# Kernel optimization log

Hardware: AMD Instinct MI355X
Metric: run time of the kernel (lower is better)

The kernel has to match this reference:

```python
import jax, jax.numpy as jnp
import numpy as np

H = 128

def _gine_conv(x, ei, ea, w1, b1, w2, b2):
    # GINEConv (eps=0): out = MLP(x + sum_{j->i} relu(x_j + e_ji))
    src, dst = ei[0], ei[1]
    m = jax.nn.relu(x[src] + ea)                      # [E, H]
    agg = jax.ops.segment_sum(m, dst, num_segments=x.shape[0])
    h = x + agg
    return jax.nn.relu(h @ w1 + b1) @ w2 + b2

def _bn(x, gamma, beta, eps=1e-5):
    # BatchNorm1d over node dim, batch statistics (training mode)
    mu = jnp.mean(x, axis=0)
    var = jnp.mean((x - mu) ** 2, axis=0)
    return gamma * (x - mu) * jax.lax.rsqrt(var + eps) + beta

def _scatter_mean(vals, ids, mask, n):
    w = mask.astype(vals.dtype)
    s = jax.ops.segment_sum(vals * w[:, None], ids, num_segments=n)
    c = jax.ops.segment_sum(w, ids, num_segments=n)
    return s / jnp.maximum(c, 1.0)[:, None]


def setup_inputs() -> dict:
    key = jax.random.key(0)
    ks = jax.random.split(key, 20)
    Nf, Nt, S, K = 320000, 100000, 20000, 16
    Ei, Eg = 1280000, 800000
    sc = 1.0 / np.sqrt(H)
    inp = {}
    inp["h_flat"] = jax.random.normal(ks[0], (Nf, H), jnp.float32)
    inp["intra_ei"] = jax.random.randint(ks[1], (2, Ei), 0, Nf, jnp.int32)
    inp["ea_flat"] = jax.random.normal(ks[2], (Ei, H), jnp.float32)
    inp["valid"] = jnp.ones((Nf,), jnp.bool_)
    inp["node_ids"] = jax.random.randint(ks[3], (Nf,), 0, Nt, jnp.int32)
    inp["N_total"] = Nt
    inp["edge_index"] = jax.random.randint(ks[4], (2, Eg), 0, Nt, jnp.int32)
    inp["edge_attr"] = jax.random.normal(ks[5], (Eg, H), jnp.float32)
    inp["sub_batch"] = jax.random.randint(ks[6], (Nf,), 0, S, jnp.int32)
    inp["S"] = S
    inp["k"] = K
    inp["root_flat_idx"] = jax.random.randint(ks[7], (S,), 0, Nf, jnp.int32)
    inp["is_root"] = jnp.zeros((Nf,), jnp.bool_)
    # parameters
    inp["local_w1"] = jax.random.normal(ks[8], (H, H), jnp.float32) * sc
    inp["local_b1"] = jnp.zeros((H,), jnp.float32)
    inp["local_w2"] = jax.random.normal(ks[9], (H, H), jnp.float32) * sc
    inp["local_b2"] = jnp.zeros((H,), jnp.float32)
    inp["local_gamma"] = jnp.ones((H,), jnp.float32)
    inp["local_beta"] = jnp.zeros((H,), jnp.float32)
    inp["global_w1"] = jax.random.normal(ks[10], (H, H), jnp.float32) * sc
    inp["global_b1"] = jnp.zeros((H,), jnp.float32)
    inp["global_w2"] = jax.random.normal(ks[11], (H, H), jnp.float32) * sc
    inp["global_b2"] = jnp.zeros((H,), jnp.float32)
    inp["global_gamma"] = jnp.ones((H,), jnp.float32)
    inp["global_beta"] = jnp.zeros((H,), jnp.float32)
    inp["skip_w"] = jax.random.normal(ks[12], (H, H), jnp.float32) * sc
    inp["skip_b"] = jnp.zeros((H,), jnp.float32)
    inp["vv_w"] = jax.random.normal(ks[13], (H, H), jnp.float32) * sc
    inp["vv_b"] = jnp.zeros((H,), jnp.float32)
    inp["kk_w"] = jax.random.normal(ks[14], (H, H), jnp.float32) * sc
    inp["kk_b"] = jnp.zeros((H,), jnp.float32)
    return inp


def reference(h_flat, intra_ei, ea_flat, valid, node_ids, N_total, edge_index, edge_attr,
              sub_batch, S, k, root_flat_idx, is_root,
              local_w1, local_b1, local_w2, local_b2, local_gamma, local_beta,
              global_w1, global_b1, global_w2, global_b2, global_gamma, global_beta,
              skip_w, skip_b, vv_w, vv_b, kk_w, kk_b):
    valid_f = valid.astype(h_flat.dtype)[:, None]
    clamped_ids = jnp.maximum(node_ids, 0)
    valid_mask = node_ids >= 0

    h_skip = (h_flat @ skip_w + skip_b) * valid_f

    h1 = _gine_conv(h_flat, intra_ei, ea_flat, local_w1, local_b1, local_w2, local_b2)
    h1 = _bn(h1, local_gamma, local_beta) * valid_f

    x_sum = _scatter_mean(h_flat, clamped_ids, valid_mask, N_total)   # [N_total, H]
    h2 = _gine_conv(x_sum, edge_index, edge_attr, global_w1, global_b1, global_w2, global_b2)
    h2 = _bn(h2, global_gamma, global_beta)[clamped_ids] * valid_f

    root_ids = node_ids[root_flat_idx]
    root_valid = root_ids >= 0
    x_vv_canonical = _scatter_mean(h_flat[root_flat_idx], jnp.maximum(root_ids, 0), root_valid, N_total)
    x_vv = (x_vv_canonical[clamped_ids] @ vv_w + vv_b) * valid_f

    x_kk = (h_flat[root_flat_idx[sub_batch]] @ kk_w + kk_b) * valid_f

    out = jax.nn.relu(h_skip + h1 + h2 + x_vv + x_kk)
    # dropout p=0.0 -> identity
    return out * valid_f
```

## Files before the change

kernel.cpp:

```cpp
#include <hip/hip_runtime.h>

#define H    128
#define HQ   32
#define TM   64
#define NT   100000
#define XS   136


typedef __attribute__((ext_vector_type(8))) short short8;
typedef __attribute__((ext_vector_type(4))) float f32x4;

static __host__ int cdiv(long a, long b) { return (int)((a + b - 1) / b); }
static __host__ char* alignp(char* p) {
    return (char*)(((uintptr_t)p + 255) & ~(uintptr_t)255);
}

__device__ inline unsigned short f2bf(float f) {
    unsigned u = __float_as_uint(f);
    unsigned r = u + 0x7FFFu + ((u >> 16) & 1u);
    return (unsigned short)(r >> 16);
}
__device__ inline float bf2f(unsigned short u) {
    return __uint_as_float((unsigned)u << 16);
}

struct WJobs { const float* src[7]; };

__global__ __launch_bounds__(256) void k_cvt_all(
    const float* __restrict__ in, unsigned short* __restrict__ out, long n8,
    WJobs wj, unsigned short* __restrict__ dstBase, int nCvt)
{
    if ((int)blockIdx.x < nCvt) {
        long i = (long)blockIdx.x * 256 + threadIdx.x;
        if (i >= n8) return;
        float4 a = ((const float4*)in)[2 * i];
        float4 b = ((const float4*)in)[2 * i + 1];
        ushort4 lo; lo.x = f2bf(a.x); lo.y = f2bf(a.y); lo.z = f2bf(a.z); lo.w = f2bf(a.w);
        ushort4 hi; hi.x = f2bf(b.x); hi.y = f2bf(b.y); hi.z = f2bf(b.z); hi.w = f2bf(b.w);
        ((ushort4*)out)[2 * i]     = lo;
        ((ushort4*)out)[2 * i + 1] = hi;
    } else {
        int b = blockIdx.x - nCvt;
        int w = b >> 4, chunk = b & 15;
        int i = chunk * 256 + threadIdx.x;
        int k = i >> 5, n4 = (i & 31) * 4;
        float4 v = ((const float4*)wj.src[w])[i];
        unsigned short* dst = dstBase + (size_t)w * H * H;
        dst[(n4 + 0) * H + k] = f2bf(v.x);
        dst[(n4 + 1) * H + k] = f2bf(v.y);
        dst[(n4 + 2) * H + k] = f2bf(v.z);
        dst[(n4 + 3) * H + k] = f2bf(v.w);
    }
}

struct CsrJobs {
    const int* ids[4];
    const int* srcarr[4];
    const int* rfi;
    int* cnt[4];
    int* rp[4];
    int* cur[4];
    int* eid[4];
    int2* pair[4];
    int  E[4];
    int  N[4];
    int  histBase[5];
    int  scanBase[5];
};

__device__ inline int csr_id(const CsrJobs& jb, int sg, int e)
{
    if (sg == 3) {
        int nid = jb.ids[2][jb.rfi[e]];
        return nid > 0 ? nid : 0;
    }
    return jb.ids[sg][e];
}

__global__ __launch_bounds__(256) void k_hist4(CsrJobs jb)
{
    int b = blockIdx.x, sg = 0;
    while (b >= jb.histBase[sg + 1]) ++sg;
    int e = (b - jb.histBase[sg]) * 256 + threadIdx.x;
    if (e < jb.E[sg]) atomicAdd(&jb.cnt[sg][csr_id(jb, sg, e)], 1);
}

__global__ __launch_bounds__(256) void k_scanA4(CsrJobs jb, int* __restrict__ parts)
{
    int b = blockIdx.x, sg = 0;
    while (b >= jb.scanBase[sg + 1]) ++sg;
    int lb = b - jb.scanBase[sg];
    const int* cnt = jb.cnt[sg];
    int* rowptr = jb.rp[sg];
    int N = jb.N[sg];
    int* partials = parts + sg * 256;

    __shared__ int lsum[256];
    int tid = threadIdx.x;
    int base = lb * 2048 + tid * 8;
    int v[8];
    int tsum = 0;
#pragma unroll
    for (int i = 0; i < 8; ++i) {
        int idx = base + i;
        int t = (idx < N) ? cnt[idx] : 0;
        v[i] = tsum;
        tsum += t;
    }
    lsum[tid] = tsum;
    __syncthreads();
    for (int off = 1; off < 256; off <<= 1) {
        int t = (tid >= off) ? lsum[tid - off] : 0;
        __syncthreads();
        lsum[tid] += t;
        __syncthreads();
    }
    int texcl = lsum[tid] - tsum;
#pragma unroll
    for (int i = 0; i < 8; ++i) {
        int idx = base + i;
        if (idx < N) rowptr[idx] = v[i] + texcl;
    }
    if (tid == 255) partials[lb] = lsum[255];
}

__global__ __launch_bounds__(256) void k_scanB4(CsrJobs jb, int* __restrict__ parts)
{
    int sg = blockIdx.x;
    int P = jb.scanBase[sg + 1] - jb.scanBase[sg];
    int* partials = parts + sg * 256;
    int* rowptr = jb.rp[sg];
    int N = jb.N[sg];

    __shared__ int lsum[256];
    int tid = threadIdx.x;
    int val = (tid < P) ? partials[tid] : 0;
    lsum[tid] = val;
    __syncthreads();
    for (int off = 1; off < 256; off <<= 1) {
        int t = (tid >= off) ? lsum[tid - off] : 0;
        __syncthreads();
        lsum[tid] += t;
        __syncthreads();
    }
    if (tid < P) partials[tid] = lsum[tid] - val;
    if (tid == 255) rowptr[N] = lsum[255];
}

__global__ __launch_bounds__(256) void k_scanC4(CsrJobs jb, const int* __restrict__ parts)
{
    int b = blockIdx.x, sg = 0;
    while (b >= jb.scanBase[sg + 1]) ++sg;
    int lb = b - jb.scanBase[sg];
    int off = parts[sg * 256 + lb];
    int N = jb.N[sg];
    int* rowptr = jb.rp[sg];
    int* cursor = jb.cur[sg];
    int base = lb * 2048;
    for (int i = threadIdx.x; i < 2048; i += 256) {
        int g = base + i;
        if (g < N) {
            int v = rowptr[g] + off;
            rowptr[g] = v;
            cursor[g] = v;
        }
    }
}

__global__ __launch_bounds__(256) void k_fillperm4(CsrJobs jb)
{
    int b = blockIdx.x, sg = 0;
    while (b >= jb.histBase[sg + 1]) ++sg;
    int e = (b - jb.histBase[sg]) * 256 + threadIdx.x;
    if (e < jb.E[sg]) {
        int pos = atomicAdd(&jb.cur[sg][csr_id(jb, sg, e)], 1);
        if (jb.srcarr[sg]) jb.pair[sg][pos] = make_int2(e, jb.srcarr[sg][e]);
        else               jb.eid[sg][pos] = e;
    }
}

__global__ __launch_bounds__(256) void k_csr_mean(
    const unsigned short* __restrict__ X, const int* __restrict__ eid,
    const int* __restrict__ rowptr, unsigned short* __restrict__ OUT, int N)
{
    int idx = blockIdx.x * 256 + threadIdx.x;
    int n = idx >> 5, l = idx & 31;
    if (n >= N) return;
    int beg = rowptr[n], end = rowptr[n + 1];
    float4 acc = {0.f, 0.f, 0.f, 0.f};
    for (int c0 = beg; c0 < end; c0 += 32) {
        int cnt = min(32, end - c0);
        int f_l = 0;
        if (l < cnt) f_l = eid[c0 + l];
        for (int j = 0; j < cnt; ++j) {
            int fi = __shfl(f_l, j, 32);
            ushort4 h = ((const ushort4*)(X + (size_t)fi * H))[l];
            acc.x += bf2f(h.x); acc.y += bf2f(h.y);
            acc.z += bf2f(h.z); acc.w += bf2f(h.w);
        }
    }
    float inv = 1.0f / fmaxf((float)(end - beg), 1.0f);
    ushort4 o;
    o.x = f2bf(acc.x * inv); o.y = f2bf(acc.y * inv);
    o.z = f2bf(acc.z * inv); o.w = f2bf(acc.w * inv);
    ((ushort4*)(OUT + (size_t)n * H))[l] = o;
}

__device__ inline void stage_x_copy(
    unsigned short* sX, const unsigned short* X1, const int* gidx,
    int r0, int M, int tid)
{
    int r = tid >> 2, q = tid & 3;
    int row = r0 + r;
    unsigned short* dst = &sX[r * XS + q * 32];
    if (row < M) {
        int sr = gidx ? gidx[row] : row;
        const ushort4* xp = (const ushort4*)(X1 + (size_t)sr * H + q * 32);
#pragma unroll
        for (int i = 0; i < 8; ++i) *(ushort4*)(dst + i * 4) = xp[i];
    } else {
#pragma unroll
        for (int i = 0; i < 8; ++i) *(ushort4*)(dst + i * 4) = ushort4{0, 0, 0, 0};
    }
}

__device__ inline void stage_wt_pre(
    unsigned short* sWT, const unsigned short* WT, int tid)
{
    for (int i = tid; i < H * HQ; i += 256) {
        int n = i >> 5, kq = i & 31;
        *(ushort4*)&sWT[n * XS + kq * 4] = ((const ushort4*)WT)[i];
    }
}

__device__ inline void stage_wt_half(
    unsigned short* sWT, const unsigned short* WT, int h, int tid)
{
    for (int i = tid; i < 64 * HQ; i += 256) {
        int n = i >> 5, kq = i & 31;
        *(ushort4*)&sWT[n * XS + kq * 4] = ((const ushort4*)WT)[h * 2048 + i];
    }
}

__global__ __launch_bounds__(256) void k_gemm(
    const unsigned short* __restrict__ X1, const int* __restrict__ gidx,
    const unsigned short* __restrict__ WT, const float* __restrict__ B,
    unsigned short* __restrict__ OUT, int M)
{
    __shared__ unsigned short sX[TM * XS];
    __shared__ unsigned short sWT[H * XS];
    __shared__ float sB[H];
    int tid = threadIdx.x;
    int r0 = blockIdx.x * TM;

    stage_x_copy(sX, X1, gidx, r0, M, tid);
    stage_wt_pre(sWT, WT, tid);
    if (tid < 32) ((float4*)sB)[tid] = ((const float4*)B)[tid];
    __syncthreads();

    int wv = tid >> 6, l = tid & 63;
    int lr = l & 15, hi = l >> 4, lk = hi * 8;

    f32x4 acc[8];
#pragma unroll
    for (int ct = 0; ct < 8; ++ct) acc[ct] = {0.f, 0.f, 0.f, 0.f};
#pragma unroll
    for (int kk = 0; kk < 4; ++kk) {
        short8 a = *(const short8*)&sX[(wv * 16 + lr) * XS + kk * 32 + lk];
#pragma unroll
        for (int ct = 0; ct < 8; ++ct) {
            short8 b = *(const short8*)&sWT[(ct * 16 + lr) * XS + kk * 32 + lk];
            acc[ct] = __builtin_amdgcn_mfma_f32_16x16x32_bf16(a, b, acc[ct], 0, 0, 0);
        }
    }

    int orow0 = r0 + wv * 16 + hi * 4;
#pragma unroll
    for (int ct = 0; ct < 8; ++ct) {
        int col = ct * 16 + lr;
        float bias = sB[col];
#pragma unroll
        for (int j = 0; j < 4; ++j) {
            int row = orow0 + j;
            if (row >= M) continue;
            OUT[(size_t)row * H + col] = f2bf(acc[ct][j] + bias);
        }
    }
}

__global__ __launch_bounds__(256) void k_mean_gemm(
    const unsigned short* __restrict__ X, const int* __restrict__ eid,
    const int* __restrict__ rowmap, const int* __restrict__ rowptr,
    const unsigned short* __restrict__ WT, const float* __restrict__ B,
    unsigned short* __restrict__ OUT, int M)
{
    __shared__ unsigned short sX[TM * XS];
    __shared__ unsigned short sWT[H * XS];
    __shared__ float sB[H];
    int tid = threadIdx.x;
    int r0 = blockIdx.x * TM;

    {
        int r = tid >> 2, q = tid & 3;
        int row = r0 + r;
        float4 m[8];
#pragma unroll
        for (int i = 0; i < 8; ++i) m[i] = {0.f, 0.f, 0.f, 0.f};
        int cnt = 0;
        if (row < M) {
            int beg = rowptr[row], end = rowptr[row + 1];
            cnt = end - beg;
            for (int j = beg; j < end; ++j) {
                int fi = rowmap[eid[j]];
                const ushort4* hp = (const ushort4*)(X + (size_t)fi * H + q * 32);
#pragma unroll
                for (int i = 0; i < 8; ++i) {
                    ushort4 v = hp[i];
                    m[i].x += bf2f(v.x); m[i].y += bf2f(v.y);
                    m[i].z += bf2f(v.z); m[i].w += bf2f(v.w);
                }
            }
        }
        float inv = 1.0f / fmaxf((float)cnt, 1.0f);
        unsigned short* dst = &sX[r * XS + q * 32];
#pragma unroll
        for (int i = 0; i < 8; ++i) {
            ushort4 b;
            b.x = f2bf(m[i].x * inv); b.y = f2bf(m[i].y * inv);
            b.z = f2bf(m[i].z * inv); b.w = f2bf(m[i].w * inv);
            *(ushort4*)(dst + i * 4) = b;
        }
    }
    stage_wt_pre(sWT, WT, tid);
    if (tid < 32) ((float4*)sB)[tid] = ((const float4*)B)[tid];
    __syncthreads();

    int wv = tid >> 6, l = tid & 63;
    int lr = l & 15, hi = l >> 4, lk = hi * 8;

    f32x4 acc[8];
#pragma unroll
    for (int ct = 0; ct < 8; ++ct) acc[ct] = {0.f, 0.f, 0.f, 0.f};
#pragma unroll
    for (int kk = 0; kk < 4; ++kk) {
        short8 a = *(const short8*)&sX[(wv * 16 + lr) * XS + kk * 32 + lk];
#pragma unroll
        for (int ct = 0; ct < 8; ++ct) {
            short8 b = *(const short8*)&sWT[(ct * 16 + lr) * XS + kk * 32 + lk];
            acc[ct] = __builtin_amdgcn_mfma_f32_16x16x32_bf16(a, b, acc[ct], 0, 0, 0);
        }
    }

    int orow0 = r0 + wv * 16 + hi * 4;
#pragma unroll
    for (int ct = 0; ct < 8; ++ct) {
        int col = ct * 16 + lr;
        float bias = sB[col];
#pragma unroll
        for (int j = 0; j < 4; ++j) {
            int row = orow0 + j;
            if (row >= M) continue;
            OUT[(size_t)row * H + col] = f2bf(acc[ct][j] + bias);
        }
    }
}

__global__ __launch_bounds__(256) void k_mlp_agg(
    const unsigned short* __restrict__ X1,
    const float* __restrict__ EA,
    const int2* __restrict__ pair,
    const int* __restrict__ rowptr,
    const unsigned short* __restrict__ W1T, const float* __restrict__ B1,
    const unsigned short* __restrict__ W2T, const float* __restrict__ B2,
    unsigned short* __restrict__ OUT, int M,
    float* __restrict__ gs, float* __restrict__ gs2)
{
    __shared__ unsigned short sX[TM * XS];
    __shared__ unsigned short sWT[64 * XS];
    __shared__ float sB1[H], sB2[H];
    __shared__ float sS[H], sS2[H];
    int tid = threadIdx.x;
    int r0 = blockIdx.x * TM;

    {
        int r = tid >> 2, q = tid & 3;
        int row = r0 + r;
        unsigned short* dst = &sX[r * XS + q * 32];
        if (row < M) {
            float4 m[8];
            const ushort4* xp = (const ushort4*)(X1 + (size_t)row * H + q * 32);
#pragma unroll
            for (int i = 0; i < 8; ++i) {
                ushort4 v = xp[i];
                m[i].x = bf2f(v.x); m[i].y = bf2f(v.y);
                m[i].z = bf2f(v.z); m[i].w = bf2f(v.w);
            }
            int beg = rowptr[row], end = rowptr[row + 1];
            int j = beg;
            for (; j + 2 <= end; j += 2) {
                int2 p0 = pair[j], p1 = pair[j + 1];
                const float4* ep0 = (const float4*)(EA + (size_t)p0.x * H) + q * 8;
                const float4* ep1 = (const float4*)(EA + (size_t)p1.x * H) + q * 8;
                const ushort4* hp0 = (const ushort4*)(X1 + (size_t)p0.y * H + q * 32);
                const ushort4* hp1 = (const ushort4*)(X1 + (size_t)p1.y * H + q * 32);
#pragma unroll
                for (int i = 0; i < 8; ++i) {
                    float4 a0 = ep0[i], a1 = ep1[i];
                    ushort4 h0 = hp0[i], h1 = hp1[i];
                    m[i].x += fmaxf(bf2f(h0.x) + a0.x, 0.f) + fmaxf(bf2f(h1.x) + a1.x, 0.f);
                    m[i].y += fmaxf(bf2f(h0.y) + a0.y, 0.f) + fmaxf(bf2f(h1.y) + a1.y, 0.f);
                    m[i].z += fmaxf(bf2f(h0.z) + a0.z, 0.f) + fmaxf(bf2f(h1.z) + a1.z, 0.f);
                    m[i].w += fmaxf(bf2f(h0.w) + a0.w, 0.f) + fmaxf(bf2f(h1.w) + a1.w, 0.f);
                }
            }
            if (j < end) {
                int2 p = pair[j];
                const float4* ep = (const float4*)(EA + (size_t)p.x * H) + q * 8;
                const ushort4* hp = (const ushort4*)(X1 + (size_t)p.y * H + q * 32);
#pragma unroll
                for (int i = 0; i < 8; ++i) {
                    float4 a = ep[i];
                    ushort4 h = hp[i];
                    m[i].x += fmaxf(bf2f(h.x) + a.x, 0.f);
                    m[i].y += fmaxf(bf2f(h.y) + a.y, 0.f);
                    m[i].z += fmaxf(bf2f(h.z) + a.z, 0.f);
                    m[i].w += fmaxf(bf2f(h.w) + a.w, 0.f);
                }
            }
#pragma unroll
            for (int i = 0; i < 8; ++i) {
                ushort4 b;
                b.x = f2bf(m[i].x); b.y = f2bf(m[i].y);
                b.z = f2bf(m[i].z); b.w = f2bf(m[i].w);
                *(ushort4*)(dst + i * 4) = b;
            }
        } else {
#pragma unroll
            for (int i = 0; i < 8; ++i) *(ushort4*)(dst + i * 4) = ushort4{0, 0, 0, 0};
        }
    }
    stage_wt_half(sWT, W1T, 0, tid);
    if (tid < 32) ((float4*)sB1)[tid] = ((const float4*)B1)[tid];
    else if (tid < 64) ((float4*)sB2)[tid - 32] = ((const float4*)B2)[tid - 32];
    if (tid >= 64 && tid < 192) { sS[tid - 64] = 0.f; sS2[tid - 64] = 0.f; }
    __syncthreads();

    int wv = tid >> 6, l = tid & 63;
    int lr = l & 15, hi = l >> 4, lk = hi * 8;
    int rloc = wv * 16 + hi * 4;

    f32x4 acc[8];
#pragma unroll
    for (int ct = 0; ct < 8; ++ct) acc[ct] = {0.f, 0.f, 0.f, 0.f};

#pragma unroll
    for (int kk = 0; kk < 4; ++kk) {
        short8 a = *(const short8*)&sX[(wv * 16 + lr) * XS + kk * 32 + lk];
#pragma unroll
        for (int ct = 0; ct < 4; ++ct) {
            short8 b = *(const short8*)&sWT[(ct * 16 + lr) * XS + kk * 32 + lk];
            acc[ct] = __builtin_amdgcn_mfma_f32_16x16x32_bf16(a, b, acc[ct], 0, 0, 0);
        }
    }
    __syncthreads();
    stage_wt_half(sWT, W1T, 1, tid);
    __syncthreads();
#pragma unroll
    for (int kk = 0; kk < 4; ++kk) {
        short8 a = *(const short8*)&sX[(wv * 16 + lr) * XS + kk * 32 + lk];
#pragma unroll
        for (int ct = 4; ct < 8; ++ct) {
            short8 b = *(const short8*)&sWT[((ct - 4) * 16 + lr) * XS + kk * 32 + lk];
            acc[ct] = __builtin_amdgcn_mfma_f32_16x16x32_bf16(a, b, acc[ct], 0, 0, 0);
        }
    }
    __syncthreads();

#pragma unroll
    for (int ct = 0; ct < 8; ++ct) {
        int c = ct * 16 + lr;
        float b1v = sB1[c];
#pragma unroll
        for (int j = 0; j < 4; ++j) {
            float v = fmaxf(acc[ct][j] + b1v, 0.f);
            int mybf = (int)f2bf(v);
            int other = __shfl_xor(mybf, 1);
            if (!(lr & 1)) {
                unsigned packed = (unsigned)(unsigned short)mybf
                                | ((unsigned)(unsigned short)other << 16);
                *(unsigned*)&sX[(rloc + j) * XS + c] = packed;
            }
        }
        acc[ct] = {0.f, 0.f, 0.f, 0.f};
    }
    stage_wt_half(sWT, W2T, 0, tid);
    __syncthreads();

#pragma unroll
    for (int kk = 0; kk < 4; ++kk) {
        short8 a = *(const short8*)&sX[(wv * 16 + lr) * XS + kk * 32 + lk];
#pragma unroll
        for (int ct = 0; ct < 4; ++ct) {
            short8 b = *(const short8*)&sWT[(ct * 16 + lr) * XS + kk * 32 + lk];
            acc[ct] = __builtin_amdgcn_mfma_f32_16x16x32_bf16(a, b, acc[ct], 0, 0, 0);
        }
    }
    __syncthreads();
    stage_wt_half(sWT, W2T, 1, tid);
    __syncthreads();
#pragma unroll
    for (int kk = 0; kk < 4; ++kk) {
        short8 a = *(const short8*)&sX[(wv * 16 + lr) * XS + kk * 32 + lk];
#pragma unroll
        for (int ct = 4; ct < 8; ++ct) {
            short8 b = *(const short8*)&sWT[((ct - 4) * 16 + lr) * XS + kk * 32 + lk];
            acc[ct] = __builtin_amdgcn_mfma_f32_16x16x32_bf16(a, b, acc[ct], 0, 0, 0);
        }
    }

    int orow0 = r0 + rloc;
#pragma unroll
    for (int ct = 0; ct < 8; ++ct) {
        int col = ct * 16 + lr;
        float b2v = sB2[col];
        float ps = 0.f, ps2 = 0.f;
#pragma unroll
        for (int j = 0; j < 4; ++j) {
            int row = orow0 + j;
            if (row >= M) continue;
            float o = acc[ct][j] + b2v;
            OUT[(size_t)row * H + col] = f2bf(o);
            ps += o; ps2 += o * o;
        }
        atomicAdd(&sS[col], ps);
        atomicAdd(&sS2[col], ps2);
    }
    __syncthreads();
    if (tid < H) {
        unsafeAtomicAdd(&gs[tid], sS[tid]);
        unsafeAtomicAdd(&gs2[tid], sS2[tid]);
    }
}

__global__ __launch_bounds__(256) void k_final_gemm(
    const unsigned short* __restrict__ Hf,
    const unsigned short* __restrict__ SKWT, const float* __restrict__ SKB,
    const unsigned short* __restrict__ h1raw, const unsigned short* __restrict__ h2raw,
    const unsigned short* __restrict__ vvy, const unsigned short* __restrict__ kky,
    const int* __restrict__ node_ids, const int* __restrict__ sub_batch,
    const float* __restrict__ stats,
    const float* __restrict__ lg, const float* __restrict__ lbe,
    const float* __restrict__ gg, const float* __restrict__ gbe,
    float n1, float n2,
    float* __restrict__ OUT, int M)
{
    __shared__ unsigned short sX[TM * XS];
    __shared__ unsigned short sWT[H * XS];
    __shared__ float sP[5 * H];
    int tid = threadIdx.x;
    int r0 = blockIdx.x * TM;

    stage_x_copy(sX, Hf, nullptr, r0, M, tid);
    stage_wt_pre(sWT, SKWT, tid);
    if (tid < H) {
        float mu = stats[tid] / n1;
        float var = stats[H + tid] / n1 - mu * mu;
        float sc = lg[tid] * rsqrtf(var + 1e-5f);
        sP[tid] = sc; sP[H + tid] = lbe[tid] - mu * sc;
        mu = stats[2 * H + tid] / n2;
        var = stats[3 * H + tid] / n2 - mu * mu;
        sc = gg[tid] * rsqrtf(var + 1e-5f);
        sP[2 * H + tid] = sc; sP[3 * H + tid] = gbe[tid] - mu * sc;
    } else if (tid < H + 32) {
        ((float4*)(sP + 4 * H))[tid - H] = ((const float4*)SKB)[tid - H];
    }
    __syncthreads();

    int wv = tid >> 6, l = tid & 63;
    int lr = l & 15, hi = l >> 4, lk = hi * 8;

    f32x4 acc[8];
#pragma unroll
    for (int ct = 0; ct < 8; ++ct) acc[ct] = {0.f, 0.f, 0.f, 0.f};
#pragma unroll
    for (int kk = 0; kk < 4; ++kk) {
        short8 a = *(const short8*)&sX[(wv * 16 + lr) * XS + kk * 32 + lk];
#pragma unroll
        for (int ct = 0; ct < 8; ++ct) {
            short8 b = *(const short8*)&sWT[(ct * 16 + lr) * XS + kk * 32 + lk];
            acc[ct] = __builtin_amdgcn_mfma_f32_16x16x32_bf16(a, b, acc[ct], 0, 0, 0);
        }
    }
    __syncthreads();

    float* sF = (float*)sWT;
    int rloc0 = wv * 16 + hi * 4;
#pragma unroll
    for (int ct = 0; ct < 8; ++ct) {
        int col = ct * 16 + lr;
        float skbv = sP[4 * H + col];
#pragma unroll
        for (int j = 0; j < 4; ++j)
            sF[(rloc0 + j) * 130 + col] = acc[ct][j] + skbv;
    }
    __syncthreads();

    {
        int r = tid >> 2, q = tid & 3;
        int row = r0 + r;
        if (row < M) {
            int nid = node_ids[row];
            size_t cid = (size_t)(nid > 0 ? nid : 0);
            size_t sb  = (size_t)sub_batch[row];
            const ushort4* h1p = (const ushort4*)(h1raw + (size_t)row * H + q * 32);
            const ushort4* h2p = (const ushort4*)(h2raw + cid * H + q * 32);
            const ushort4* vvp = (const ushort4*)(vvy + cid * H + q * 32);
            const ushort4* kkp = (const ushort4*)(kky + sb * H + q * 32);
            float* op = OUT + (size_t)row * H + q * 32;
            const float* fr = &sF[r * 130 + q * 32];
#pragma unroll
            for (int i = 0; i < 8; ++i) {
                ushort4 a = h1p[i], b = h2p[i], c = vvp[i], d = kkp[i];
                int cb = q * 32 + i * 4;
                float4 o;
                o.x = fr[i * 4 + 0] + bf2f(a.x) * sP[cb + 0] + sP[H + cb + 0]
                    + bf2f(b.x) * sP[2 * H + cb + 0] + sP[3 * H + cb + 0]
                    + bf2f(c.x) + bf2f(d.x);
                o.y = fr[i * 4 + 1] + bf2f(a.y) * sP[cb + 1] + sP[H + cb + 1]
                    + bf2f(b.y) * sP[2 * H + cb + 1] + sP[3 * H + cb + 1]
                    + bf2f(c.y) + bf2f(d.y);
                o.z = fr[i * 4 + 2] + bf2f(a.z) * sP[cb + 2] + sP[H + cb + 2]
                    + bf2f(b.z) * sP[2 * H + cb + 2] + sP[3 * H + cb + 2]
                    + bf2f(c.z) + bf2f(d.z);
                o.w = fr[i * 4 + 3] + bf2f(a.w) * sP[cb + 3] + sP[H + cb + 3]
                    + bf2f(b.w) * sP[2 * H + cb + 3] + sP[3 * H + cb + 3]
                    + bf2f(c.w) + bf2f(d.w);
                o.x = fmaxf(o.x, 0.f); o.y = fmaxf(o.y, 0.f);
                o.z = fmaxf(o.z, 0.f); o.w = fmaxf(o.w, 0.f);
                ((float4*)op)[i] = o;
            }
        }
    }
}

extern "C" void kernel_launch(void* const* d_in, const int* in_sizes, int n_in,
                              void* d_out, int out_size, void* d_ws, size_t ws_size,
                              hipStream_t stream)
{
    const float* h_flat        = (const float*)d_in[0];
    const int*   intra_ei      = (const int*)d_in[1];
    const float* ea_flat       = (const float*)d_in[2];
    const int*   node_ids      = (const int*)d_in[4];
    const int*   edge_index    = (const int*)d_in[6];
    const float* edge_attr     = (const float*)d_in[7];
    const int*   sub_batch     = (const int*)d_in[8];
    const int*   root_flat_idx = (const int*)d_in[11];
    const float* lw1 = (const float*)d_in[13];
    const float* lb1 = (const float*)d_in[14];
    const float* lw2 = (const float*)d_in[15];
    const float* lb2 = (const float*)d_in[16];
    const float* lg  = (const float*)d_in[17];
    const float* lbe = (const float*)d_in[18];
    const float* gw1 = (const float*)d_in[19];
    const float* gb1 = (const float*)d_in[20];
    const float* gw2 = (const float*)d_in[21];
    const float* gb2 = (const float*)d_in[22];
    const float* gg  = (const float*)d_in[23];
    const float* gbe = (const float*)d_in[24];
    const float* skw = (const float*)d_in[25];
    const float* skb = (const float*)d_in[26];
    const float* vvw = (const float*)d_in[27];
    const float* vvb = (const float*)d_in[28];
    const float* kkw = (const float*)d_in[29];
    const float* kkb = (const float*)d_in[30];

    const int Nf = in_sizes[0] / H;
    const int Ei = in_sizes[2] / H;
    const int Eg = in_sizes[7] / H;
    const int S  = in_sizes[11];

    char* w = (char*)d_ws;
    unsigned short* hbf  = (unsigned short*)w; w += (size_t)Nf * H * 2;
    unsigned short* buf1 = (unsigned short*)w; w += (size_t)Nf * H * 2;
    unsigned short* xsum = (unsigned short*)w; w += (size_t)NT * H * 2;
    unsigned short* buf2 = (unsigned short*)w; w += (size_t)NT * H * 2;
    unsigned short* vvy  = (unsigned short*)w; w += (size_t)NT * H * 2;
    unsigned short* kbuf = (unsigned short*)w; w += (size_t)S * H * 2;
    unsigned short* wtb  = (unsigned short*)w; w += (size_t)7 * H * H * 2;
    w = alignp(w);
    int* cntAll = (int*)w; w += ((size_t)Nf + 3 * (size_t)NT) * 4;
    float* stats = (float*)w; w += 4 * H * 4;
    w = alignp(w);
    int* rpA  = (int*)w; w += ((size_t)Nf + 1) * 4;  w = alignp(w);
    int* rpB  = (int*)w; w += ((size_t)NT + 1) * 4;  w = alignp(w);
    int* rpC  = (int*)w; w += ((size_t)NT + 1) * 4;  w = alignp(w);
    int* rpD  = (int*)w; w += ((size_t)NT + 1) * 4;  w = alignp(w);
    int* curA = (int*)w; w += (size_t)Nf * 4;
    int* curB = (int*)w; w += (size_t)NT * 4;
    int* curC = (int*)w; w += (size_t)NT * 4;
    int* curD = (int*)w; w += (size_t)NT * 4;
    int* eidC = (int*)w; w += (size_t)Nf * 4;
    int* eidD = (int*)w; w += (size_t)S * 4;
    w = alignp(w);
    int2* pairA = (int2*)w; w += (size_t)Ei * 8;
    int2* pairB = (int2*)w; w += (size_t)Eg * 8;
    int* parts = (int*)w; w += 4 * 256 * 4;
    int* cntA = cntAll;
    int* cntB = cntA + Nf;
    int* cntC = cntB + NT;
    int* cntD = cntC + NT;

    hipMemsetAsync(cntAll, 0, ((size_t)Nf + 3 * (size_t)NT) * 4 + 4 * H * 4, stream);

    WJobs wj;
    wj.src[0] = lw1; wj.src[1] = lw2; wj.src[2] = gw1; wj.src[3] = gw2;
    wj.src[4] = skw; wj.src[5] = vvw; wj.src[6] = kkw;
    int nCvt = cdiv((long)Nf * H / 8, 256);
    k_cvt_all<<<nCvt + 7 * 16, 256, 0, stream>>>(
        h_flat, hbf, (long)Nf * H / 8, wj, wtb, nCvt);

    CsrJobs jb;
    jb.ids[0] = intra_ei + Ei;  jb.ids[1] = edge_index + Eg;
    jb.ids[2] = node_ids;       jb.ids[3] = nullptr;
    jb.srcarr[0] = intra_ei;    jb.srcarr[1] = edge_index;
    jb.srcarr[2] = nullptr;     jb.srcarr[3] = nullptr;
    jb.rfi = root_flat_idx;
    jb.cnt[0] = cntA; jb.cnt[1] = cntB; jb.cnt[2] = cntC; jb.cnt[3] = cntD;
    jb.rp[0]  = rpA;  jb.rp[1]  = rpB;  jb.rp[2]  = rpC;  jb.rp[3]  = rpD;
    jb.cur[0] = curA; jb.cur[1] = curB; jb.cur[2] = curC; jb.cur[3] = curD;
    jb.eid[0] = nullptr; jb.eid[1] = nullptr; jb.eid[2] = eidC; jb.eid[3] = eidD;
    jb.pair[0] = pairA; jb.pair[1] = pairB; jb.pair[2] = nullptr; jb.pair[3] = nullptr;
    jb.E[0] = Ei; jb.E[1] = Eg; jb.E[2] = Nf; jb.E[3] = S;
    jb.N[0] = Nf; jb.N[1] = NT; jb.N[2] = NT; jb.N[3] = NT;
    jb.histBase[0] = 0;
    for (int i = 0; i < 4; ++i) jb.histBase[i + 1] = jb.histBase[i] + cdiv(jb.E[i], 256);
    jb.scanBase[0] = 0;
    for (int i = 0; i < 4; ++i) jb.scanBase[i + 1] = jb.scanBase[i] + cdiv(jb.N[i], 2048);

    k_hist4<<<jb.histBase[4], 256, 0, stream>>>(jb);
    k_scanA4<<<jb.scanBase[4], 256, 0, stream>>>(jb, parts);
    k_scanB4<<<4, 256, 0, stream>>>(jb, parts);
    k_scanC4<<<jb.scanBase[4], 256, 0, stream>>>(jb, parts);
    k_fillperm4<<<jb.histBase[4], 256, 0, stream>>>(jb);

    k_csr_mean<<<cdiv((long)NT * 32, 256), 256, 0, stream>>>(
        hbf, eidC, rpC, xsum, NT);

    k_mlp_agg<<<cdiv(Nf, TM), 256, 0, stream>>>(
        hbf, ea_flat, pairA, rpA,
        wtb + 0 * H * H, lb1, wtb + 1 * H * H, lb2,
        buf1, Nf, stats, stats + H);
    k_mlp_agg<<<cdiv(NT, TM), 256, 0, stream>>>(
        xsum, edge_attr, pairB, rpB,
        wtb + 2 * H * H, gb1, wtb + 3 * H * H, gb2,
        buf2, NT, stats + 2 * H, stats + 3 * H);

    k_mean_gemm<<<cdiv(NT, TM), 256, 0, stream>>>(
        hbf, eidD, root_flat_idx, rpD, wtb + 5 * H * H, vvb, vvy, NT);
    k_gemm<<<cdiv(S, TM), 256, 0, stream>>>(hbf, root_flat_idx,
                                            wtb + 6 * H * H, kkb, kbuf, S);

    k_final_gemm<<<cdiv(Nf, TM), 256, 0, stream>>>(
        hbf, wtb + 4 * H * H, skb, buf1, buf2, vvy, kbuf, node_ids, sub_batch,
        stats, lg, lbe, gg, gbe, (float)Nf, (float)NT, (float*)d_out, Nf);
}
```

Before: 1.173 ms.

## Split edge aggregation out of MLP kernel into warp-per-node gather kernel

Edge aggregation moves out of the fused MLP kernel into a separate kernel that gives each destination node 32 lanes. Each lane reads a contiguous float4 or ushort4 slice of the edge-attribute and source rows, which gives coalesced 512-byte row reads. The MLP kernel then only sums x and the stored aggregate before its GEMMs. Before, four threads per row walked the edge list serially inside the GEMM block, giving poor memory parallelism and load imbalance. The cost is an extra bf16 round trip of the aggregate through global memory, two extra launches, and one more bf16 rounding of x+agg. The aggregate is written in place into buf1/buf2, which the MLP reads and then overwrites with its output. Each block reads and writes only its own rows, so this looks safe.

```diff
diff --git a/kernel.cpp b/kernel.cpp
--- a/kernel.cpp
+++ b/kernel.cpp
@@ -179,6 +179,36 @@
     }
 }
 
+__global__ __launch_bounds__(256) void k_edge_agg(
+    const unsigned short* __restrict__ X, const float* __restrict__ EA,
+    const int2* __restrict__ pair, const int* __restrict__ rowptr,
+    unsigned short* __restrict__ OUT, int N)
+{
+    int idx = blockIdx.x * 256 + threadIdx.x;
+    int n = idx >> 5, l = idx & 31;
+    if (n >= N) return;
+    int beg = rowptr[n], end = rowptr[n + 1];
+    float4 acc = {0.f, 0.f, 0.f, 0.f};
+    for (int c0 = beg; c0 < end; c0 += 32) {
+        int cnt = min(32, end - c0);
+        int2 p_l = make_int2(0, 0);
+        if (l < cnt) p_l = pair[c0 + l];
+        for (int j = 0; j < cnt; ++j) {
+            int e = __shfl(p_l.x, j, 32);
+            int s = __shfl(p_l.y, j, 32);
+            float4 a = ((const float4*)(EA + (size_t)e * H))[l];
+            ushort4 h = ((const ushort4*)(X + (size_t)s * H))[l];
+            acc.x += fmaxf(bf2f(h.x) + a.x, 0.f);
+            acc.y += fmaxf(bf2f(h.y) + a.y, 0.f);
+            acc.z += fmaxf(bf2f(h.z) + a.z, 0.f);
+            acc.w += fmaxf(bf2f(h.w) + a.w, 0.f);
+        }
+    }
+    ushort4 o;
+    o.x = f2bf(acc.x); o.y = f2bf(acc.y); o.z = f2bf(acc.z); o.w = f2bf(acc.w);
+    ((ushort4*)(OUT + (size_t)n * H))[l] = o;
+}
+
 __global__ __launch_bounds__(256) void k_csr_mean(
     const unsigned short* __restrict__ X, const int* __restrict__ eid,
     const int* __restrict__ rowptr, unsigned short* __restrict__ OUT, int N)
@@ -224,6 +254,32 @@
     }
 }
 
+__device__ inline void stage_x_sum(
+    unsigned short* sX, const unsigned short* X1, const unsigned short* X2,
+    int r0, int M, int tid)
+{
+    int r = tid >> 2, q = tid & 3;
+    int row = r0 + r;
+    unsigned short* dst = &sX[r * XS + q * 32];
+    if (row < M) {
+        const ushort4* xp = (const ushort4*)(X1 + (size_t)row * H + q * 32);
+        const ushort4* yp = (const ushort4*)(X2 + (size_t)row * H + q * 32);
+#pragma unroll
+        for (int i = 0; i < 8; ++i) {
+            ushort4 a = xp[i], b = yp[i];
+            ushort4 o;
+            o.x = f2bf(bf2f(a.x) + bf2f(b.x));
+            o.y = f2bf(bf2f(a.y) + bf2f(b.y));
+            o.z = f2bf(bf2f(a.z) + bf2f(b.z));
+            o.w = f2bf(bf2f(a.w) + bf2f(b.w));
+            *(ushort4*)(dst + i * 4) = o;
+        }
+    } else {
+#pragma unroll
+        for (int i = 0; i < 8; ++i) *(ushort4*)(dst + i * 4) = ushort4{0, 0, 0, 0};
+    }
+}
+
 __device__ inline void stage_wt_pre(
     unsigned short* sWT, const unsigned short* WT, int tid)
 {
@@ -365,11 +421,8 @@
     }
 }
 
-__global__ __launch_bounds__(256) void k_mlp_agg(
-    const unsigned short* __restrict__ X1,
-    const float* __restrict__ EA,
-    const int2* __restrict__ pair,
-    const int* __restrict__ rowptr,
+__global__ __launch_bounds__(256) void k_mlp(
+    const unsigned short* __restrict__ X1, const unsigned short* __restrict__ AGG,
     const unsigned short* __restrict__ W1T, const float* __restrict__ B1,
     const unsigned short* __restrict__ W2T, const float* __restrict__ B2,
     unsigned short* __restrict__ OUT, int M,
@@ -382,63 +435,7 @@
     int tid = threadIdx.x;
     int r0 = blockIdx.x * TM;
 
-    {
-        int r = tid >> 2, q = tid & 3;
-        int row = r0 + r;
-        unsigned short* dst = &sX[r * XS + q * 32];
-        if (row < M) {
-            float4 m[8];
-            const ushort4* xp = (const ushort4*)(X1 + (size_t)row * H + q * 32);
-#pragma unroll
-            for (int i = 0; i < 8; ++i) {
-                ushort4 v = xp[i];
-                m[i].x = bf2f(v.x); m[i].y = bf2f(v.y);
-                m[i].z = bf2f(v.z); m[i].w = bf2f(v.w);
-            }
-            int beg = rowptr[row], end = rowptr[row + 1];
-            int j = beg;
-            for (; j + 2 <= end; j += 2) {
-                int2 p0 = pair[j], p1 = pair[j + 1];
-                const float4* ep0 = (const float4*)(EA + (size_t)p0.x * H) + q * 8;
-                const float4* ep1 = (const float4*)(EA + (size_t)p1.x * H) + q * 8;
-                const ushort4* hp0 = (const ushort4*)(X1 + (size_t)p0.y * H + q * 32);
-                const ushort4* hp1 = (const ushort4*)(X1 + (size_t)p1.y * H + q * 32);
-#pragma unroll
-                for (int i = 0; i < 8; ++i) {
-                    float4 a0 = ep0[i], a1 = ep1[i];
-                    ushort4 h0 = hp0[i], h1 = hp1[i];
-                    m[i].x += fmaxf(bf2f(h0.x) + a0.x, 0.f) + fmaxf(bf2f(h1.x) + a1.x, 0.f);
-                    m[i].y += fmaxf(bf2f(h0.y) + a0.y, 0.f) + fmaxf(bf2f(h1.y) + a1.y, 0.f);
-                    m[i].z += fmaxf(bf2f(h0.z) + a0.z, 0.f) + fmaxf(bf2f(h1.z) + a1.z, 0.f);
-                    m[i].w += fmaxf(bf2f(h0.w) + a0.w, 0.f) + fmaxf(bf2f(h1.w) + a1.w, 0.f);
-                }
-            }
-            if (j < end) {
-                int2 p = pair[j];
-                const float4* ep = (const float4*)(EA + (size_t)p.x * H) + q * 8;
-                const ushort4* hp = (const ushort4*)(X1 + (size_t)p.y * H + q * 32);
-#pragma unroll
-                for (int i = 0; i < 8; ++i) {
-                    float4 a = ep[i];
-                    ushort4 h = hp[i];
-                    m[i].x += fmaxf(bf2f(h.x) + a.x, 0.f);
-                    m[i].y += fmaxf(bf2f(h.y) + a.y, 0.f);
-                    m[i].z += fmaxf(bf2f(h.z) + a.z, 0.f);
-                    m[i].w += fmaxf(bf2f(h.w) + a.w, 0.f);
-                }
-            }
-#pragma unroll
-            for (int i = 0; i < 8; ++i) {
-                ushort4 b;
-                b.x = f2bf(m[i].x); b.y = f2bf(m[i].y);
-                b.z = f2bf(m[i].z); b.w = f2bf(m[i].w);
-                *(ushort4*)(dst + i * 4) = b;
-            }
-        } else {
-#pragma unroll
-            for (int i = 0; i < 8; ++i) *(ushort4*)(dst + i * 4) = ushort4{0, 0, 0, 0};
-        }
-    }
+    stage_x_sum(sX, X1, AGG, r0, M, tid);
     stage_wt_half(sWT, W1T, 0, tid);
     if (tid < 32) ((float4*)sB1)[tid] = ((const float4*)B1)[tid];
     else if (tid < 64) ((float4*)sB2)[tid - 32] = ((const float4*)B2)[tid - 32];
@@ -745,14 +742,16 @@
 
     k_csr_mean<<<cdiv((long)NT * 32, 256), 256, 0, stream>>>(
         hbf, eidC, rpC, xsum, NT);
-
-    k_mlp_agg<<<cdiv(Nf, TM), 256, 0, stream>>>(
-        hbf, ea_flat, pairA, rpA,
-        wtb + 0 * H * H, lb1, wtb + 1 * H * H, lb2,
+    k_edge_agg<<<cdiv((long)Nf * 32, 256), 256, 0, stream>>>(
+        hbf, ea_flat, pairA, rpA, buf1, Nf);
+    k_edge_agg<<<cdiv((long)NT * 32, 256), 256, 0, stream>>>(
+        xsum, edge_attr, pairB, rpB, buf2, NT);
+
+    k_mlp<<<cdiv(Nf, TM), 256, 0, stream>>>(
+        hbf, buf1, wtb + 0 * H * H, lb1, wtb + 1 * H * H, lb2,
         buf1, Nf, stats, stats + H);
-    k_mlp_agg<<<cdiv(NT, TM), 256, 0, stream>>>(
-        xsum, edge_attr, pairB, rpB,
-        wtb + 2 * H * H, gb1, wtb + 3 * H * H, gb2,
+    k_mlp<<<cdiv(NT, TM), 256, 0, stream>>>(
+        xsum, buf2, wtb + 2 * H * H, gb1, wtb + 3 * H * H, gb2,
         buf2, NT, stats + 2 * H, stats + 3 * H);
 
     k_mean_gemm<<<cdiv(NT, TM), 256, 0, stream>>>(
```

New measurement: 1.168 ms. About the same (-0.4%).
